# Kernel tuning notes

Hardware: AMD Instinct MI355X
Metric: run time of the kernel (lower is better)

## Reference

```python
import jax, jax.numpy as jnp
import numpy as np

NUM_BIN = 64
NUM_CAT_GROUPS = 64
INTERVALS_PER_CAT = 16
NUM_CAT_CH = NUM_CAT_GROUPS * INTERVALS_PER_CAT  # 1024
NUM_NUM = 4096
K_VAL = 16
BATCH = 16384
IN1 = NUM_BIN + NUM_CAT_CH + NUM_NUM           # 5184 (input1)
IN2 = NUM_BIN + NUM_CAT_GROUPS + NUM_NUM // K_VAL  # 384 (input2)


def setup_inputs() -> dict:
    key = jax.random.key(0)
    k1, k2, k3, k4, k5 = jax.random.split(key, 5)
    return {
        "input_linear": jax.random.normal(k1, (BATCH, IN1, 1), dtype=jnp.float32),
        # grouped conv1d kernel=1, groups=C  ==  per-channel scale + bias
        "w1": jax.random.normal(k2, (IN1,), dtype=jnp.float32) * 0.1,
        "b1": jax.random.normal(k3, (IN1,), dtype=jnp.float32) * 0.1,
        "w2": jax.random.normal(k4, (IN2,), dtype=jnp.float32) * 0.1,
        "b2": jax.random.normal(k5, (IN2,), dtype=jnp.float32) * 0.1,
        "K": K_VAL,
        "train_size": BATCH,
        "num_cat_variable": NUM_CAT_CH,
        "num_num_variable": NUM_NUM,
        "num_bin_variable": NUM_BIN,
        "vectorized_cate_col_name_num_list": jnp.full((NUM_CAT_GROUPS,), INTERVALS_PER_CAT, dtype=jnp.int32),
    }


def reference(input_linear, w1, b1, w2, b2, K, train_size, num_cat_variable,
              num_num_variable, num_bin_variable, vectorized_cate_col_name_num_list):
    # layer_piecewise: Conv1d(C, C, 1, groups=C) == per-channel affine
    y1 = input_linear * w1[None, :, None] + b1[None, :, None]  # [B, IN1, 1]

    y1_bin = y1[:, :num_bin_variable, :]                                          # [B, 64, 1]
    y1_cat = y1[:, num_bin_variable:num_bin_variable + num_cat_variable, :]       # [B, 1024, 1]
    y1_num = y1[:, num_bin_variable + num_cat_variable:, :]                       # [B, 4096, 1]

    # irregular categorical aggregation: variable-size contiguous channel groups
    seg_ids = jnp.repeat(jnp.arange(NUM_CAT_GROUPS),
                         vectorized_cate_col_name_num_list,
                         total_repeat_length=NUM_CAT_CH)
    temp_cat = jax.ops.segment_sum(y1_cat.transpose(1, 0, 2), seg_ids,
                                   num_segments=NUM_CAT_GROUPS).transpose(1, 0, 2)  # [B, 64, 1]

    # numeric aggregation: group j sums channels j*K .. j*K+K-1 (index[i::K] pattern)
    G = num_num_variable // K
    temp_num = y1_num.reshape(train_size, G, K, 1).sum(axis=2)  # [B, 256, 1]

    y1_agg = jnp.concatenate([y1_bin, temp_cat, temp_num], axis=1)  # [B, IN2, 1]

    # layer_summation: another per-channel affine
    y2 = y1_agg * w2[None, :, None] + b2[None, :, None]
    return jnp.sum(y2, axis=1)  # [B, 1]
```

## Files before the change

### kernel.cpp

```cpp
#include <hip/hip_runtime.h>

constexpr int NUM_BIN  = 64;
constexpr int NUM_CAT  = 1024;
constexpr int NUM_NUM  = 4096;
constexpr int IN1_C    = NUM_BIN + NUM_CAT + NUM_NUM;
constexpr int IN2_C    = 64 + 64 + 256;
constexpr int BATCH_C  = 16384;
constexpr int NF4      = IN1_C / 4;

typedef float f32x4 __attribute__((ext_vector_type(4)));

__global__ __launch_bounds__(256) void pwl_fused(
    const float* __restrict__ x,  const float* __restrict__ w1,
    const float* __restrict__ b1, const float* __restrict__ w2,
    const float* __restrict__ b2, float* __restrict__ out)
{
    __shared__ f32x4 wlds[NF4];
    __shared__ float red[4];

    const int tid  = threadIdx.x;
    const int lane = tid & 63;
    const int wid  = tid >> 6;
    const int row  = blockIdx.x * 4 + wid;

    float* wl = (float*)wlds;

    float partial = 0.f;
    #pragma unroll
    for (int i = 0; i < 20; ++i) {
        const int c = tid + 256 * i;
        int j;
        if (c < NUM_BIN)                j = c;
        else if (c < NUM_BIN + NUM_CAT) j = NUM_BIN + ((c - NUM_BIN) >> 4);
        else                            j = 128 + ((c - NUM_BIN - NUM_CAT) >> 4);
        const float w2j = w2[j];
        wl[c]    = w1[c] * w2j;
        partial += b1[c] * w2j;
    }
    if (tid < 64) {
        const int c = 5120 + tid;
        const float w2j = w2[128 + ((c - NUM_BIN - NUM_CAT) >> 4)];
        wl[c]    = w1[c] * w2j;
        partial += b1[c] * w2j;
    }
    partial += b2[tid] + ((tid < IN2_C - 256) ? b2[tid + 256] : 0.f);

    for (int off = 32; off > 0; off >>= 1)
        partial += __shfl_down(partial, off, 64);
    if (lane == 0) red[wid] = partial;
    __syncthreads();

    const f32x4* __restrict__ xr = (const f32x4*)(x + (size_t)row * IN1_C);

    float s0 = 0.f, s1 = 0.f, s2 = 0.f, s3 = 0.f;
    #pragma unroll
    for (int k = 0; k < 20; k += 4) {
        const int i0 = lane + 64 * k;
        f32x4 a0 = xr[i0];
        f32x4 a1 = xr[i0 + 64];
        f32x4 a2 = xr[i0 + 128];
        f32x4 a3 = xr[i0 + 192];
        f32x4 w0 = wlds[i0];
        f32x4 w1v = wlds[i0 + 64];
        f32x4 w2v = wlds[i0 + 128];
        f32x4 w3v = wlds[i0 + 192];
        s0 += a0.x * w0.x + a0.y * w0.y + a0.z * w0.z + a0.w * w0.w;
        s1 += a1.x * w1v.x + a1.y * w1v.y + a1.z * w1v.z + a1.w * w1v.w;
        s2 += a2.x * w2v.x + a2.y * w2v.y + a2.z * w2v.z + a2.w * w2v.w;
        s3 += a3.x * w3v.x + a3.y * w3v.y + a3.z * w3v.z + a3.w * w3v.w;
    }
    if (lane < 16) {
        f32x4 a = xr[lane + 1280];
        f32x4 w = wlds[lane + 1280];
        s0 += a.x * w.x + a.y * w.y + a.z * w.z + a.w * w.w;
    }

    float sum = (s0 + s1) + (s2 + s3);
    for (int off = 32; off > 0; off >>= 1)
        sum += __shfl_down(sum, off, 64);

    if (lane == 0)
        out[row] = sum + (red[0] + red[1]) + (red[2] + red[3]);
}

extern "C" void kernel_launch(void* const* d_in, const int* in_sizes, int n_in,
                              void* d_out, int out_size, void* d_ws, size_t ws_size,
                              hipStream_t stream)
{
    const float* x  = (const float*)d_in[0];
    const float* w1 = (const float*)d_in[1];
    const float* b1 = (const float*)d_in[2];
    const float* w2 = (const float*)d_in[3];
    const float* b2 = (const float*)d_in[4];
    float* out = (float*)d_out;

    const int blocks = BATCH_C / 4;
    pwl_fused<<<blocks, 256, 0, stream>>>(x, w1, b1, w2, b2, out);
}
```

Before: 60.94 us.

## Keep folded weights in per-wave registers instead of shared memory

Each wave now computes the combined w1*w2 weights for its own lanes straight into a 21-entry register array, which removes the shared-memory staging, the LDS reads in the dot-product loop and the __syncthreads barrier. The constant bias term is reduced inside each wave and broadcast with a shuffle. The cost is that all four waves redundantly load and compute the weights, which adds register pressure (84 floats per thread) and extra global/L2 traffic for w1, b1 and w2.

Measured after the change: 76.12 us. +24.9%, slower.

```diff
diff --git a/kernel.cpp b/kernel.cpp
--- a/kernel.cpp
+++ b/kernel.cpp
@@ -1,54 +1,57 @@
 #include <hip/hip_runtime.h>
 
-constexpr int NUM_BIN  = 64;
-constexpr int NUM_CAT  = 1024;
-constexpr int NUM_NUM  = 4096;
-constexpr int IN1_C    = NUM_BIN + NUM_CAT + NUM_NUM;
-constexpr int IN2_C    = 64 + 64 + 256;
-constexpr int BATCH_C  = 16384;
-constexpr int NF4      = IN1_C / 4;
+constexpr int IN1_C   = 5184;
+constexpr int BATCH_C = 16384;
 
 typedef float f32x4 __attribute__((ext_vector_type(4)));
 
-__global__ __launch_bounds__(256) void pwl_fused(
+__device__ __forceinline__ float dot4(f32x4 a, f32x4 b) {
+    return a.x * b.x + a.y * b.y + a.z * b.z + a.w * b.w;
+}
+
+__global__ __launch_bounds__(256) void pwl_reg(
     const float* __restrict__ x,  const float* __restrict__ w1,
     const float* __restrict__ b1, const float* __restrict__ w2,
     const float* __restrict__ b2, float* __restrict__ out)
 {
-    __shared__ f32x4 wlds[NF4];
-    __shared__ float red[4];
+    const int lane = threadIdx.x & 63;
+    const int row  = blockIdx.x * 4 + (threadIdx.x >> 6);
 
-    const int tid  = threadIdx.x;
-    const int lane = tid & 63;
-    const int wid  = tid >> 6;
-    const int row  = blockIdx.x * 4 + wid;
+    const f32x4* __restrict__ w1v4 = (const f32x4*)w1;
+    const f32x4* __restrict__ b1v4 = (const f32x4*)b1;
 
-    float* wl = (float*)wlds;
-
+    f32x4 wv[21];
     float partial = 0.f;
     #pragma unroll
-    for (int i = 0; i < 20; ++i) {
-        const int c = tid + 256 * i;
-        int j;
-        if (c < NUM_BIN)                j = c;
-        else if (c < NUM_BIN + NUM_CAT) j = NUM_BIN + ((c - NUM_BIN) >> 4);
-        else                            j = 128 + ((c - NUM_BIN - NUM_CAT) >> 4);
-        const float w2j = w2[j];
-        wl[c]    = w1[c] * w2j;
-        partial += b1[c] * w2j;
+    for (int k = 0; k < 21; ++k) {
+        const int c4 = (k < 20) ? (lane + 64 * k) : ((lane & 15) + 1280);
+        const f32x4 a  = w1v4[c4];
+        const f32x4 bb = b1v4[c4];
+        f32x4 wj;
+        #pragma unroll
+        for (int e = 0; e < 4; ++e) {
+            const int c = 4 * c4 + e;
+            int j;
+            if (c < 64)        j = c;
+            else if (c < 1088) j = 64  + ((c - 64)   >> 4);
+            else               j = 128 + ((c - 1088) >> 4);
+            wj[e] = w2[j];
+        }
+        f32x4 ew = a * wj;
+        float pb = dot4(bb, wj);
+        if (k == 20 && lane >= 16) {
+            ew.x = 0.f; ew.y = 0.f; ew.z = 0.f; ew.w = 0.f;
+            pb = 0.f;
+        }
+        wv[k] = ew;
+        partial += pb;
     }
-    if (tid < 64) {
-        const int c = 5120 + tid;
-        const float w2j = w2[128 + ((c - NUM_BIN - NUM_CAT) >> 4)];
-        wl[c]    = w1[c] * w2j;
-        partial += b1[c] * w2j;
-    }
-    partial += b2[tid] + ((tid < IN2_C - 256) ? b2[tid + 256] : 0.f);
-
+    #pragma unroll
+    for (int i = 0; i < 6; ++i)
+        partial += b2[lane + 64 * i];
     for (int off = 32; off > 0; off >>= 1)
         partial += __shfl_down(partial, off, 64);
-    if (lane == 0) red[wid] = partial;
-    __syncthreads();
+    const float cst = __shfl(partial, 0, 64);
 
     const f32x4* __restrict__ xr = (const f32x4*)(x + (size_t)row * IN1_C);
 
@@ -60,27 +63,21 @@
         f32x4 a1 = xr[i0 + 64];
         f32x4 a2 = xr[i0 + 128];
         f32x4 a3 = xr[i0 + 192];
-        f32x4 w0 = wlds[i0];
-        f32x4 w1v = wlds[i0 + 64];
-        f32x4 w2v = wlds[i0 + 128];
-        f32x4 w3v = wlds[i0 + 192];
-        s0 += a0.x * w0.x + a0.y * w0.y + a0.z * w0.z + a0.w * w0.w;
-        s1 += a1.x * w1v.x + a1.y * w1v.y + a1.z * w1v.z + a1.w * w1v.w;
-        s2 += a2.x * w2v.x + a2.y * w2v.y + a2.z * w2v.z + a2.w * w2v.w;
-        s3 += a3.x * w3v.x + a3.y * w3v.y + a3.z * w3v.z + a3.w * w3v.w;
+        s0 += dot4(a0, wv[k]);
+        s1 += dot4(a1, wv[k + 1]);
+        s2 += dot4(a2, wv[k + 2]);
+        s3 += dot4(a3, wv[k + 3]);
     }
-    if (lane < 16) {
-        f32x4 a = xr[lane + 1280];
-        f32x4 w = wlds[lane + 1280];
-        s0 += a.x * w.x + a.y * w.y + a.z * w.z + a.w * w.w;
+    {
+        f32x4 ar = xr[(lane & 15) + 1280];
+        s0 += dot4(ar, wv[20]);
     }
 
     float sum = (s0 + s1) + (s2 + s3);
     for (int off = 32; off > 0; off >>= 1)
         sum += __shfl_down(sum, off, 64);
 
-    if (lane == 0)
-        out[row] = sum + (red[0] + red[1]) + (red[2] + red[3]);
+    if (lane == 0) out[row] = sum + cst;
 }
 
 extern "C" void kernel_launch(void* const* d_in, const int* in_sizes, int n_in,
@@ -95,5 +92,5 @@
     float* out = (float*)d_out;
 
     const int blocks = BATCH_C / 4;
-    pwl_fused<<<blocks, 256, 0, stream>>>(x, w1, b1, w2, b2, out);
+    pwl_reg<<<blocks, 256, 0, stream>>>(x, w1, b1, w2, b2, out);
 }
```
